# Performance work log

Hardware: AMD Instinct MI355X
Metric: run time of the kernel (lower is better)

Reference implementation:

```python
import jax, jax.numpy as jnp
import numpy as np

EPS = 1e-5  # torch LayerNorm default

def _std(x):
    # standardize over the last 3 (tensor-feature) modes, biased variance like torch LayerNorm
    mu = jnp.mean(x, axis=(-3, -2, -1), keepdims=True)
    var = jnp.mean(jnp.square(x - mu), axis=(-3, -2, -1), keepdims=True)
    return (x - mu) * jax.lax.rsqrt(var + EPS)

def setup_inputs() -> dict:
    key = jax.random.key(0)
    ks = jax.random.split(key, 12)
    T, B = 512, 16
    a = b = c = 16          # input tensor modes (4096 features)
    ha = hb = hc = 8        # hidden tensor modes (512 features)
    G = 3                   # gates: r, z, n
    f32 = jnp.float32
    return {
        "x": jax.random.normal(ks[0], (T, B, a, b, c), f32),
        "h0": jnp.zeros((B, ha, hb, hc), f32),
        # input-to-hidden TCL3D factors + rank-1 bias + LN affines (stacked over 3 gates)
        "W_fa": jax.random.normal(ks[1], (G, a, ha), f32),
        "W_fb": jax.random.normal(ks[2], (G, b, hb), f32),
        "W_fc": jax.random.normal(ks[3], (G, c, hc), f32),
        "W_ba": jax.random.normal(ks[4], (G, ha), f32),
        "W_bb": jax.random.normal(ks[5], (G, hb), f32),
        "W_bc": jax.random.normal(ks[6], (G, hc), f32),
        "W_lnin_w": jnp.ones((G, a, b, c), f32),
        "W_lnin_b": jnp.zeros((G, a, b, c), f32),
        "W_lnout_w": jnp.ones((G, ha, hb, hc), f32),
        "W_lnout_b": jnp.zeros((G, ha, hb, hc), f32),
        # hidden-to-hidden TCL3D factors + rank-1 bias + LN affines
        "U_fa": jax.random.normal(ks[7], (G, ha, ha), f32),
        "U_fb": jax.random.normal(ks[8], (G, hb, hb), f32),
        "U_fc": jax.random.normal(ks[9], (G, hc, hc), f32),
        "U_ba": jax.random.normal(ks[10], (G, ha), f32),
        "U_bb": jax.random.normal(ks[11], (G, hb), f32),
        "U_bc": jax.random.normal(jax.random.fold_in(key, 99), (G, hc), f32),
        "U_lnin_w": jnp.ones((G, ha, hb, hc), f32),
        "U_lnin_b": jnp.zeros((G, ha, hb, hc), f32),
        "U_lnout_w": jnp.ones((G, ha, hb, hc), f32),
        "U_lnout_b": jnp.zeros((G, ha, hb, hc), f32),
    }

def reference(x, h0, W_fa, W_fb, W_fc, W_ba, W_bb, W_bc,
              W_lnin_w, W_lnin_b, W_lnout_w, W_lnout_b,
              U_fa, U_fb, U_fc, U_ba, U_bb, U_bc,
              U_lnin_w, U_lnin_b, U_lnout_w, U_lnout_b):
    # --- input-to-hidden TCL3D for all 3 gates, batched over time (no h dependence) ---
    xh = _std(x)                                                  # [T,B,a,b,c]
    xg = xh[None] * W_lnin_w[:, None, None] + W_lnin_b[:, None, None]  # [3,T,B,a,b,c]
    Wx = jnp.einsum('gtnabc,gad,gbe,gcf->gtndef', xg, W_fa, W_fb, W_fc)
    Wx = Wx + (W_ba[:, None, None, :, None, None]
               * W_bb[:, None, None, None, :, None]
               * W_bc[:, None, None, None, None, :])              # rank-1 bias
    Wx = _std(Wx) * W_lnout_w[:, None, None] + W_lnout_b[:, None, None]
    Wx = jnp.swapaxes(Wx, 0, 1)                                   # [T,3,B,ha,hb,hc]

    Ub = (U_ba[:, None, :, None, None]
          * U_bb[:, None, None, :, None]
          * U_bc[:, None, None, None, :])                         # [3,1,ha,hb,hc]

    def step(h, wx):
        # hidden-to-hidden TCL3D for all 3 gates
        hh = _std(h)                                              # [B,ha,hb,hc]
        hg = hh[None] * U_lnin_w[:, None] + U_lnin_b[:, None]     # [3,B,ha,hb,hc]
        Uh = jnp.einsum('gndef,gdp,geq,gfr->gnpqr', hg, U_fa, U_fb, U_fc) + Ub
        Uh = _std(Uh) * U_lnout_w[:, None] + U_lnout_b[:, None]
        r = jax.nn.sigmoid(wx[0] + Uh[0])
        z = jax.nn.sigmoid(wx[1] + Uh[1])
        n = jnp.tanh(wx[2] + r * Uh[2])
        h_new = (1.0 - z) * n + z * h
        return h_new, h_new

    _, outs = jax.lax.scan(step, h0, Wx)                          # [T,B,ha,hb,hc]
    return outs
```

## Files before the change

kernel.cpp:

```cpp
#include <hip/hip_runtime.h>

#define EPSV 1e-5f

#define KEEPV(x) asm volatile("" : "+v"(x))
#define KEEPS(x) asm volatile("" : "+s"(x))

#define DPP_XADD(v, ctrl)                                                  \
    v += __int_as_float(__builtin_amdgcn_update_dpp(                       \
        0, __float_as_int(v), ctrl, 0xF, 0xF, false))

__device__ __forceinline__ float wave_allsum(float v) {
    DPP_XADD(v, 0x128);
    DPP_XADD(v, 0x124);
    DPP_XADD(v, 0x122);
    DPP_XADD(v, 0x121);
    DPP_XADD(v, 0x142);
    DPP_XADD(v, 0x143);
    return __int_as_float(__builtin_amdgcn_readlane(__float_as_int(v), 63));
}

__device__ __forceinline__ void bar_lds() {
    asm volatile("s_waitcnt lgkmcnt(0)\n\ts_barrier" ::: "memory");
}

__global__ __launch_bounds__(256) void wx_kernel(
    const float* __restrict__ x,
    const float* __restrict__ Wfa, const float* __restrict__ Wfb,
    const float* __restrict__ Wfc,
    const float* __restrict__ Wba, const float* __restrict__ Wbb,
    const float* __restrict__ Wbc,
    const float* __restrict__ lniw, const float* __restrict__ lnib,
    const float* __restrict__ lnow, const float* __restrict__ lnob,
    float* __restrict__ wxo)
{
    __shared__ float Xs[4096];
    __shared__ float S1[2048];
    __shared__ float S2[1024];
    __shared__ float baS[24], bbS[24], bcS[24];
    __shared__ float red[16];

    const int tid  = threadIdx.x;
    const int wid  = tid >> 6, lane = tid & 63;
    const size_t tb = blockIdx.x;
    const float* xp = x + tb * 4096;

    float s = 0.f, s2 = 0.f;
    for (int i = tid; i < 4096; i += 256) {
        float v = xp[i];
        Xs[i] = v;
        s += v; s2 += v * v;
    }
    if (tid < 24) { baS[tid] = Wba[tid]; bbS[tid] = Wbb[tid]; bcS[tid] = Wbc[tid]; }

    __syncthreads();
    #pragma unroll
    for (int off = 32; off > 0; off >>= 1) {
        s  += __shfl_down(s,  off);
        s2 += __shfl_down(s2, off);
    }
    if (lane == 0) { red[wid] = s; red[8 + wid] = s2; }
    __syncthreads();
    s  = red[0] + red[1] + red[2] + red[3];
    s2 = red[8] + red[9] + red[10] + red[11];
    const float muX = s * (1.f / 4096.f);
    const float rsX = rsqrtf(fmaxf(s2 * (1.f / 4096.f) - muX * muX, 0.f) + EPSV);

    const int qh = __builtin_amdgcn_readfirstlane(tid >> 7);
    const int rh = __builtin_amdgcn_readfirstlane(tid >> 6);

    for (int g = 0; g < 3; ++g) {
        {
            float acc[8] = {0,0,0,0,0,0,0,0};
            const int rest = tid;
            const float* lw = lniw + g * 4096;
            const float* lb = lnib + g * 4096;
            #pragma unroll
            for (int m = 0; m < 16; ++m) {
                const float xn = (Xs[m*256 + rest] - muX) * rsX;
                const float xv = fmaf(xn, lw[m*256 + rest], lb[m*256 + rest]);
                #pragma unroll
                for (int p = 0; p < 8; ++p)
                    acc[p] = fmaf(xv, Wfa[(g*16 + m)*8 + p], acc[p]);
            }
            #pragma unroll
            for (int p = 0; p < 8; ++p)
                S1[p*256 + (rest ^ (p << 3))] = acc[p];
        }
        __syncthreads();
        {
            float acc[4] = {0,0,0,0};
            const int rest2 = tid & 127;
            const int c2 = rest2 >> 3, p2 = rest2 & 7;
            #pragma unroll
            for (int m = 0; m < 16; ++m) {
                const float xv = S1[p2*256 + (((m << 4) | c2) ^ (p2 << 3))];
                #pragma unroll
                for (int j = 0; j < 4; ++j)
                    acc[j] = fmaf(xv, Wfb[(g*16 + m)*8 + qh*4 + j], acc[j]);
            }
            #pragma unroll
            for (int j = 0; j < 4; ++j) {
                const int q = qh*4 + j;
                S2[q*128 + (rest2 ^ (q << 3))] = acc[j];
            }
        }
        __syncthreads();
        float v0, v1; int idx0;
        {
            float acc[2] = {0, 0};
            const int rest3 = tid & 63;
            const int q3 = rest3 & 7, pp = rest3 >> 3;
            #pragma unroll
            for (int m = 0; m < 16; ++m) {
                const float xv = S2[q3*128 + (((m << 3) | pp) ^ (q3 << 3))];
                #pragma unroll
                for (int j = 0; j < 2; ++j)
                    acc[j] = fmaf(xv, Wfc[(g*16 + m)*8 + rh*2 + j], acc[j]);
            }
            const float bpq = baS[g*8 + pp] * bbS[g*8 + q3];
            v0 = acc[0] + bpq * bcS[g*8 + rh*2 + 0];
            v1 = acc[1] + bpq * bcS[g*8 + rh*2 + 1];
            idx0 = rest3 * 8 + rh * 2;
        }
        float t = v0 + v1, t2 = v0*v0 + v1*v1;
        __syncthreads();
        #pragma unroll
        for (int off = 32; off > 0; off >>= 1) {
            t  += __shfl_down(t,  off);
            t2 += __shfl_down(t2, off);
        }
        if (lane == 0) { red[wid] = t; red[8 + wid] = t2; }
        __syncthreads();
        t  = red[0] + red[1] + red[2] + red[3];
        t2 = red[8] + red[9] + red[10] + red[11];
        const float mu  = t * (1.f / 512.f);
        const float var = fmaxf(t2 * (1.f / 512.f) - mu * mu, 0.f);
        const float rs  = rsqrtf(var + EPSV);
        float* wp = wxo + (tb * 3 + g) * 512;
        const float2 lw2 = *(const float2*)(lnow + g*512 + idx0);
        const float2 lb2 = *(const float2*)(lnob + g*512 + idx0);
        float2 o2;
        o2.x = fmaf((v0 - mu) * rs, lw2.x, lb2.x);
        o2.y = fmaf((v1 - mu) * rs, lw2.y, lb2.y);
        *(float2*)(wp + idx0) = o2;
    }
}

__global__ __launch_bounds__(192, 1) void scan_kernel(
    const float* __restrict__ wx,
    const float* __restrict__ h0,
    const float* __restrict__ Ufa, const float* __restrict__ Ufb,
    const float* __restrict__ Ufc,
    const float* __restrict__ Uba, const float* __restrict__ Ubb,
    const float* __restrict__ Ubc,
    const float* __restrict__ lniw, const float* __restrict__ lnib,
    const float* __restrict__ lnow, const float* __restrict__ lnob,
    float* __restrict__ out,
    int T, int B)
{
    const int n    = blockIdx.x;
    const int tid  = threadIdx.x;
    const int lane = tid & 63;
    const int gu   = __builtin_amdgcn_readfirstlane(tid >> 6);

    __shared__ float hgS[3][576];
    __shared__ float T1S[3][576];
    __shared__ float T2S[3][576];
    __shared__ float UhS[2][3][576];

    float wA[64], wB[64], wC[64];
    #pragma unroll
    for (int i = 0; i < 64; ++i) {
        wA[i] = __uint_as_float(__builtin_amdgcn_readfirstlane(
                    __float_as_uint(Ufa[gu*64 + i])));
        KEEPS(wA[i]);
    }
    #pragma unroll
    for (int i = 0; i < 64; ++i) { wB[i] = Ufb[gu*64 + i]; KEEPV(wB[i]); }
    #pragma unroll
    for (int i = 0; i < 64; ++i) { wC[i] = Ufc[gu*64 + i]; KEEPV(wC[i]); }

    float lnw[8], lnb[8], low8[8], lob8[8], ubias[8];
    {
        const int p_ = lane >> 3, q_ = lane & 7;
        const float bpq = Uba[gu*8 + p_] * Ubb[gu*8 + q_];
        #pragma unroll
        for (int k = 0; k < 8; ++k) {
            lnw[k]   = lniw[gu*512 + lane*8 + k];
            lnb[k]   = lnib[gu*512 + lane*8 + k];
            low8[k]  = lnow[gu*512 + lane*8 + k];
            lob8[k]  = lnob[gu*512 + lane*8 + k];
            ubias[k] = bpq * Ubc[gu*8 + k];
        }
    }

    const int wbase = lane;
    const int rbase = (lane & 7) * 72 + (lane >> 3);

    float hv[8];
    {
        const float4 a = *(const float4*)(h0 + n*512 + lane*8);
        const float4 b = *(const float4*)(h0 + n*512 + lane*8 + 4);
        hv[0]=a.x; hv[1]=a.y; hv[2]=a.z; hv[3]=a.w;
        hv[4]=b.x; hv[5]=b.y; hv[6]=b.z; hv[7]=b.w;
    }

    float uo[8];
    float pf[3][8];

#define LOADWX(TT)                                                         \
    {                                                                      \
        const float* base_ = wx + (((size_t)(TT) * B + n) * 3) * 512       \
                             + lane * 8;                                   \
        _Pragma("unroll")                                                  \
        for (int gg = 0; gg < 3; ++gg) {                                   \
            const float4 A_ = *(const float4*)(base_ + gg*512);            \
            const float4 B_ = *(const float4*)(base_ + gg*512 + 4);        \
            pf[gg][0]=A_.x; pf[gg][1]=A_.y; pf[gg][2]=A_.z; pf[gg][3]=A_.w;\
            pf[gg][4]=B_.x; pf[gg][5]=B_.y; pf[gg][6]=B_.z; pf[gg][7]=B_.w;\
        }                                                                  \
    }

#define WR8(BUFROW, V)                                                     \
    {                                                                      \
        float* p0_ = (BUFROW) + wbase;                                     \
        float* p1_ = p0_ + 288;                                            \
        p0_[0] = V[0]; p0_[72] = V[1]; p0_[144] = V[2]; p0_[216] = V[3];   \
        p1_[0] = V[4]; p1_[72] = V[5]; p1_[144] = V[6]; p1_[216] = V[7];   \
    }

#define RD8(BUFROW, V)                                                     \
    {                                                                      \
        const float* q_ = (BUFROW) + rbase;                                \
        V[0] = q_[0];  V[1] = q_[8];  V[2] = q_[16]; V[3] = q_[24];        \
        V[4] = q_[32]; V[5] = q_[40]; V[6] = q_[48]; V[7] = q_[56];        \
    }

#define RD8W(BUFROW, V)                                                    \
    {                                                                      \
        const float* q0_ = (BUFROW) + wbase;                               \
        const float* q1_ = q0_ + 288;                                      \
        V[0] = q0_[0]; V[1] = q0_[72]; V[2] = q0_[144]; V[3] = q0_[216];   \
        V[4] = q1_[0]; V[5] = q1_[72]; V[6] = q1_[144]; V[7] = q1_[216];   \
    }

#define PIPELINE(PARN)                                                     \
    {                                                                      \
        float sA = 0.f, sB = 0.f;                                          \
        _Pragma("unroll")                                                  \
        for (int k = 0; k < 8; ++k) { sA += hv[k]; sB += hv[k]*hv[k]; }    \
        sA = wave_allsum(sA); sB = wave_allsum(sB);                        \
        const float mu_ = sA * (1.f/512.f);                                \
        const float rs_ = rsqrtf(fmaxf(sB*(1.f/512.f) - mu_*mu_, 0.f)      \
                                 + EPSV);                                  \
        float hg_[8];                                                      \
        _Pragma("unroll")                                                  \
        for (int k = 0; k < 8; ++k)                                        \
            hg_[k] = fmaf((hv[k]-mu_)*rs_, lnw[k], lnb[k]);                \
        WR8(hgS[gu], hg_)                                                  \
        float xv_[8], a_[8];                                               \
        _Pragma("unroll") for (int k = 0; k < 8; ++k) a_[k] = 0.f;         \
        RD8(hgS[gu], xv_)                                                  \
        _Pragma("unroll")                                                  \
        for (int m = 0; m < 8; ++m)                                        \
            _Pragma("unroll")                                              \
            for (int q = 0; q < 8; ++q)                                    \
                a_[q] = fmaf(xv_[m], wA[m*8 + q], a_[q]);                  \
        WR8(T1S[gu], a_)                                                   \
        RD8(T1S[gu], xv_)                                                  \
        _Pragma("unroll") for (int k = 0; k < 8; ++k) a_[k] = 0.f;         \
        _Pragma("unroll")                                                  \
        for (int m = 0; m < 8; ++m)                                        \
            _Pragma("unroll")                                              \
            for (int q = 0; q < 8; ++q)                                    \
                a_[q] = fmaf(xv_[m], wB[m*8 + q], a_[q]);                  \
        WR8(T2S[gu], a_)                                                   \
        RD8(T2S[gu], xv_)                                                  \
        _Pragma("unroll") for (int k = 0; k < 8; ++k) a_[k] = 0.f;         \
        _Pragma("unroll")                                                  \
        for (int m = 0; m < 8; ++m)                                        \
            _Pragma("unroll")                                              \
            for (int q = 0; q < 8; ++q)                                    \
                a_[q] = fmaf(xv_[m], wC[m*8 + q], a_[q]);                  \
        float sC = 0.f, sD = 0.f;                                          \
        _Pragma("unroll")                                                  \
        for (int k = 0; k < 8; ++k) {                                      \
            a_[k] += ubias[k]; sC += a_[k]; sD += a_[k]*a_[k];             \
        }                                                                  \
        sC = wave_allsum(sC); sD = wave_allsum(sD);                        \
        const float mu2_ = sC * (1.f/512.f);                               \
        const float rs2_ = rsqrtf(fmaxf(sD*(1.f/512.f) - mu2_*mu2_, 0.f)   \
                                  + EPSV);                                 \
        _Pragma("unroll")                                                  \
        for (int k = 0; k < 8; ++k)                                        \
            uo[k] = fmaf((a_[k]-mu2_)*rs2_, low8[k], lob8[k]);             \
        WR8(UhS[PARN][gu], uo)                                             \
    }

#define COMBINE(PARC, TT)                                                  \
    {                                                                      \
        float ur[8], uz[8], un[8];                                         \
        if (gu == 0) {                                                     \
            _Pragma("unroll")                                              \
            for (int k = 0; k < 8; ++k) ur[k] = uo[k];                     \
            RD8W(UhS[PARC][1], uz)                                         \
            RD8W(UhS[PARC][2], un)                                         \
        } else if (gu == 1) {                                              \
            _Pragma("unroll")                                              \
            for (int k = 0; k < 8; ++k) uz[k] = uo[k];                     \
            RD8W(UhS[PARC][0], ur)                                         \
            RD8W(UhS[PARC][2], un)                                         \
        } else {                                                           \
            _Pragma("unroll")                                              \
            for (int k = 0; k < 8; ++k) un[k] = uo[k];                     \
            RD8W(UhS[PARC][0], ur)                                         \
            RD8W(UhS[PARC][1], uz)                                         \
        }                                                                  \
        _Pragma("unroll")                                                  \
        for (int k = 0; k < 8; ++k) {                                      \
            const float er_ = __expf(-(pf[0][k] + ur[k]));                 \
            const float r_  = __builtin_amdgcn_rcpf(1.f + er_);            \
            const float ez_ = __expf(-(pf[1][k] + uz[k]));                 \
            const float z_  = __builtin_amdgcn_rcpf(1.f + ez_);            \
            const float e2_ = __expf(2.f * (pf[2][k] + r_ * un[k]));       \
            const float nn_ = 1.f - 2.f*__builtin_amdgcn_rcpf(e2_ + 1.f);  \
            hv[k] = (1.f - z_)*nn_ + z_*hv[k];                             \
        }                                                                  \
        if (gu == 0) {                                                     \
            float* op_ = out + ((size_t)(TT) * B + n) * 512 + lane*8;      \
            *(float4*)op_     = make_float4(hv[0], hv[1], hv[2], hv[3]);   \
            *(float4*)(op_+4) = make_float4(hv[4], hv[5], hv[6], hv[7]);   \
        }                                                                  \
    }

    LOADWX(0);
    PIPELINE(0);

    for (int t = 0; t < T; t += 2) {
        bar_lds();
        COMBINE(0, t)
        if (t + 1 < T) {
            LOADWX(t + 1);
            PIPELINE(1)
        }
        bar_lds();
        if (t + 1 < T) COMBINE(1, t + 1)
        if (t + 2 < T) {
            LOADWX(t + 2);
            PIPELINE(0)
        }
    }
#undef LOADWX
#undef WR8
#undef RD8
#undef RD8W
#undef PIPELINE
#undef COMBINE
}

extern "C" void kernel_launch(void* const* d_in, const int* in_sizes, int n_in,
                              void* d_out, int out_size, void* d_ws, size_t ws_size,
                              hipStream_t stream)
{
    const float* x    = (const float*)d_in[0];
    const float* h0   = (const float*)d_in[1];
    const float* Wfa  = (const float*)d_in[2];
    const float* Wfb  = (const float*)d_in[3];
    const float* Wfc  = (const float*)d_in[4];
    const float* Wba  = (const float*)d_in[5];
    const float* Wbb  = (const float*)d_in[6];
    const float* Wbc  = (const float*)d_in[7];
    const float* Wliw = (const float*)d_in[8];
    const float* Wlib = (const float*)d_in[9];
    const float* Wlow = (const float*)d_in[10];
    const float* Wlob = (const float*)d_in[11];
    const float* Ufa  = (const float*)d_in[12];
    const float* Ufb  = (const float*)d_in[13];
    const float* Ufc  = (const float*)d_in[14];
    const float* Uba  = (const float*)d_in[15];
    const float* Ubb  = (const float*)d_in[16];
    const float* Ubc  = (const float*)d_in[17];
    const float* Uliw = (const float*)d_in[18];
    const float* Ulib = (const float*)d_in[19];
    const float* Ulow = (const float*)d_in[20];
    const float* Ulob = (const float*)d_in[21];

    const int B = in_sizes[1] / 512;
    const int T = in_sizes[0] / (B * 4096);

    float* wxws = (float*)d_ws;
    float* out  = (float*)d_out;

    wx_kernel<<<T * B, 256, 0, stream>>>(x, Wfa, Wfb, Wfc, Wba, Wbb, Wbc,
                                         Wliw, Wlib, Wlow, Wlob, wxws);
    scan_kernel<<<B, 192, 0, stream>>>(wxws, h0, Ufa, Ufb, Ufc, Uba, Ubb, Ubc,
                                       Uliw, Ulib, Ulow, Ulob, out, T, B);
}
```

Baseline: 812.2 us.

## Split each gate's recurrent contraction across two waves in the scan kernel

```diff
diff --git a/kernel.cpp b/kernel.cpp
--- a/kernel.cpp
+++ b/kernel.cpp
@@ -3,7 +3,6 @@
 #define EPSV 1e-5f
 
 #define KEEPV(x) asm volatile("" : "+v"(x))
-#define KEEPS(x) asm volatile("" : "+s"(x))
 
 #define DPP_XADD(v, ctrl)                                                  \
     v += __int_as_float(__builtin_amdgcn_update_dpp(                       \
@@ -146,7 +145,7 @@
     }
 }
 
-__global__ __launch_bounds__(192, 1) void scan_kernel(
+__global__ __launch_bounds__(384, 1) void scan_kernel(
     const float* __restrict__ wx,
     const float* __restrict__ h0,
     const float* __restrict__ Ufa, const float* __restrict__ Ufb,
@@ -161,22 +160,24 @@
     const int n    = blockIdx.x;
     const int tid  = threadIdx.x;
     const int lane = tid & 63;
-    const int gu   = __builtin_amdgcn_readfirstlane(tid >> 6);
+    const int wid  = __builtin_amdgcn_readfirstlane(tid >> 6);
+    const int gu   = wid >> 1;
+    const int ju   = wid & 1;
 
     __shared__ float hgS[3][576];
     __shared__ float T1S[3][576];
     __shared__ float T2S[3][576];
     __shared__ float UhS[2][3][576];
 
-    float wA[64], wB[64], wC[64];
+    float sA[32], sB[32];
     #pragma unroll
-    for (int i = 0; i < 64; ++i) {
-        wA[i] = __uint_as_float(__builtin_amdgcn_readfirstlane(
-                    __float_as_uint(Ufa[gu*64 + i])));
-        KEEPS(wA[i]);
-    }
-    #pragma unroll
-    for (int i = 0; i < 64; ++i) { wB[i] = Ufb[gu*64 + i]; KEEPV(wB[i]); }
+    for (int m = 0; m < 8; ++m)
+        #pragma unroll
+        for (int qq = 0; qq < 4; ++qq) {
+            sA[m*4 + qq] = Ufa[gu*64 + m*8 + ju*4 + qq];
+            sB[m*4 + qq] = Ufb[gu*64 + m*8 + ju*4 + qq];
+        }
+    float wC[64];
     #pragma unroll
     for (int i = 0; i < 64; ++i) { wC[i] = Ufc[gu*64 + i]; KEEPV(wC[i]); }
 
@@ -221,12 +222,10 @@
         }                                                                  \
     }
 
-#define WR8(BUFROW, V)                                                     \
-    {                                                                      \
-        float* p0_ = (BUFROW) + wbase;                                     \
-        float* p1_ = p0_ + 288;                                            \
+#define WR4(BUFROW, V)                                                     \
+    {                                                                      \
+        float* p0_ = (BUFROW) + ju*288 + wbase;                            \
         p0_[0] = V[0]; p0_[72] = V[1]; p0_[144] = V[2]; p0_[216] = V[3];   \
-        p1_[0] = V[4]; p1_[72] = V[5]; p1_[144] = V[6]; p1_[216] = V[7];   \
     }
 
 #define RD8(BUFROW, V)                                                     \
@@ -244,57 +243,67 @@
         V[4] = q1_[0]; V[5] = q1_[72]; V[6] = q1_[144]; V[7] = q1_[216];   \
     }
 
-#define PIPELINE(PARN)                                                     \
-    {                                                                      \
-        float sA = 0.f, sB = 0.f;                                          \
-        _Pragma("unroll")                                                  \
-        for (int k = 0; k < 8; ++k) { sA += hv[k]; sB += hv[k]*hv[k]; }    \
-        sA = wave_allsum(sA); sB = wave_allsum(sB);                        \
-        const float mu_ = sA * (1.f/512.f);                                \
-        const float rs_ = rsqrtf(fmaxf(sB*(1.f/512.f) - mu_*mu_, 0.f)      \
+#define PIPE(PARN)                                                         \
+    {                                                                      \
+                                \
+        float s0_ = 0.f, s1_ = 0.f;                                        \
+        _Pragma("unroll")                                                  \
+        for (int k = 0; k < 8; ++k) { s0_ += hv[k]; s1_ += hv[k]*hv[k]; }  \
+        s0_ = wave_allsum(s0_); s1_ = wave_allsum(s1_);                    \
+        const float mu_ = s0_ * (1.f/512.f);                               \
+        const float rs_ = rsqrtf(fmaxf(s1_*(1.f/512.f) - mu_*mu_, 0.f)     \
                                  + EPSV);                                  \
-        float hg_[8];                                                      \
+        float hg_[4];                                                      \
+        _Pragma("unroll")                                                  \
+        for (int kk = 0; kk < 4; ++kk) {                                   \
+            const int k = ju*4 + kk;                                       \
+            hg_[kk] = fmaf((hv[k]-mu_)*rs_, lnw[k], lnb[k]);               \
+        }                                                                  \
+        WR4(hgS[gu], hg_)                                                  \
+        bar_lds();                                   \
+        float xv_[8], a4_[4];                                              \
+        RD8(hgS[gu], xv_)                                                  \
+        _Pragma("unroll") for (int kk = 0; kk < 4; ++kk) a4_[kk] = 0.f;    \
+        _Pragma("unroll")                                                  \
+        for (int m = 0; m < 8; ++m)                                        \
+            _Pragma("unroll")                                              \
+            for (int qq = 0; qq < 4; ++qq)                                 \
+                a4_[qq] = fmaf(xv_[m], sA[m*4 + qq], a4_[qq]);             \
+        WR4(T1S[gu], a4_)                                                  \
+        bar_lds();                                   \
+        RD8(T1S[gu], xv_)                                                  \
+        _Pragma("unroll") for (int kk = 0; kk < 4; ++kk) a4_[kk] = 0.f;    \
+        _Pragma("unroll")                                                  \
+        for (int m = 0; m < 8; ++m)                                        \
+            _Pragma("unroll")                                              \
+            for (int qq = 0; qq < 4; ++qq)                                 \
+                a4_[qq] = fmaf(xv_[m], sB[m*4 + qq], a4_[qq]);             \
+        WR4(T2S[gu], a4_)                                                  \
+        bar_lds();                                   \
+        RD8(T2S[gu], xv_)                                                  \
+        float a8_[8];                                                      \
+        _Pragma("unroll") for (int k = 0; k < 8; ++k) a8_[k] = 0.f;        \
+        _Pragma("unroll")                                                  \
+        for (int m = 0; m < 8; ++m)                                        \
+            _Pragma("unroll")                                              \
+            for (int r = 0; r < 8; ++r)                                    \
+                a8_[r] = fmaf(xv_[m], wC[m*8 + r], a8_[r]);                \
+        float s2_ = 0.f, s3_ = 0.f;                                        \
+        _Pragma("unroll")                                                  \
+        for (int k = 0; k < 8; ++k) {                                      \
+            a8_[k] += ubias[k]; s2_ += a8_[k]; s3_ += a8_[k]*a8_[k];       \
+        }                                                                  \
+        s2_ = wave_allsum(s2_); s3_ = wave_allsum(s3_);                    \
+        const float mu2_ = s2_ * (1.f/512.f);                              \
+        const float rs2_ = rsqrtf(fmaxf(s3_*(1.f/512.f) - mu2_*mu2_, 0.f)  \
+                                  + EPSV);                                 \
         _Pragma("unroll")                                                  \
         for (int k = 0; k < 8; ++k)                                        \
-            hg_[k] = fmaf((hv[k]-mu_)*rs_, lnw[k], lnb[k]);                \
-        WR8(hgS[gu], hg_)                                                  \
-        float xv_[8], a_[8];                                               \
-        _Pragma("unroll") for (int k = 0; k < 8; ++k) a_[k] = 0.f;         \
-        RD8(hgS[gu], xv_)                                                  \
-        _Pragma("unroll")                                                  \
-        for (int m = 0; m < 8; ++m)                                        \
-            _Pragma("unroll")                                              \
-            for (int q = 0; q < 8; ++q)                                    \
-                a_[q] = fmaf(xv_[m], wA[m*8 + q], a_[q]);                  \
-        WR8(T1S[gu], a_)                                                   \
-        RD8(T1S[gu], xv_)                                                  \
-        _Pragma("unroll") for (int k = 0; k < 8; ++k) a_[k] = 0.f;         \
-        _Pragma("unroll")                                                  \
-        for (int m = 0; m < 8; ++m)                                        \
-            _Pragma("unroll")                                              \
-            for (int q = 0; q < 8; ++q)                                    \
-                a_[q] = fmaf(xv_[m], wB[m*8 + q], a_[q]);                  \
-        WR8(T2S[gu], a_)                                                   \
-        RD8(T2S[gu], xv_)                                                  \
-        _Pragma("unroll") for (int k = 0; k < 8; ++k) a_[k] = 0.f;         \
-        _Pragma("unroll")                                                  \
-        for (int m = 0; m < 8; ++m)                                        \
-            _Pragma("unroll")                                              \
-            for (int q = 0; q < 8; ++q)                                    \
-                a_[q] = fmaf(xv_[m], wC[m*8 + q], a_[q]);                  \
-        float sC = 0.f, sD = 0.f;                                          \
-        _Pragma("unroll")                                                  \
-        for (int k = 0; k < 8; ++k) {                                      \
-            a_[k] += ubias[k]; sC += a_[k]; sD += a_[k]*a_[k];             \
-        }                                                                  \
-        sC = wave_allsum(sC); sD = wave_allsum(sD);                        \
-        const float mu2_ = sC * (1.f/512.f);                               \
-        const float rs2_ = rsqrtf(fmaxf(sD*(1.f/512.f) - mu2_*mu2_, 0.f)   \
-                                  + EPSV);                                 \
-        _Pragma("unroll")                                                  \
-        for (int k = 0; k < 8; ++k)                                        \
-            uo[k] = fmaf((a_[k]-mu2_)*rs2_, low8[k], lob8[k]);             \
-        WR8(UhS[PARN][gu], uo)                                             \
+            uo[k] = fmaf((a8_[k]-mu2_)*rs2_, low8[k], lob8[k]);            \
+        float uh_[4];                                                      \
+        _Pragma("unroll")                                                  \
+        for (int kk = 0; kk < 4; ++kk) uh_[kk] = uo[ju*4 + kk];            \
+        WR4(UhS[PARN][gu], uh_)                                            \
     }
 
 #define COMBINE(PARC, TT)                                                  \
@@ -326,7 +335,7 @@
             const float nn_ = 1.f - 2.f*__builtin_amdgcn_rcpf(e2_ + 1.f);  \
             hv[k] = (1.f - z_)*nn_ + z_*hv[k];                             \
         }                                                                  \
-        if (gu == 0) {                                                     \
+        if (wid == 0) {                                                    \
             float* op_ = out + ((size_t)(TT) * B + n) * 512 + lane*8;      \
             *(float4*)op_     = make_float4(hv[0], hv[1], hv[2], hv[3]);   \
             *(float4*)(op_+4) = make_float4(hv[4], hv[5], hv[6], hv[7]);   \
@@ -334,27 +343,27 @@
     }
 
     LOADWX(0);
-    PIPELINE(0);
+    PIPE(0);
 
     for (int t = 0; t < T; t += 2) {
         bar_lds();
         COMBINE(0, t)
         if (t + 1 < T) {
             LOADWX(t + 1);
-            PIPELINE(1)
+            PIPE(1)
         }
         bar_lds();
         if (t + 1 < T) COMBINE(1, t + 1)
         if (t + 2 < T) {
             LOADWX(t + 2);
-            PIPELINE(0)
+            PIPE(0)
         }
     }
 #undef LOADWX
-#undef WR8
+#undef WR4
 #undef RD8
 #undef RD8W
-#undef PIPELINE
+#undef PIPE
 #undef COMBINE
 }
 
@@ -393,6 +402,6 @@
 
     wx_kernel<<<T * B, 256, 0, stream>>>(x, Wfa, Wfb, Wfc, Wba, Wbb, Wbc,
                                          Wliw, Wlib, Wlow, Wlob, wxws);
-    scan_kernel<<<B, 192, 0, stream>>>(wxws, h0, Ufa, Ufb, Ufc, Uba, Ubb, Ubc,
+    scan_kernel<<<B, 384, 0, stream>>>(wxws, h0, Ufa, Ufb, Ufc, Uba, Ubb, Ubc,
                                        Uliw, Ulib, Ulow, Ulob, out, T, B);
 }
```

New measurement: 1.451 ms. +78.6%, slower.
